# Kernel tuning notes

Measured on AMD Instinct MI355X. Metric: run time of the kernel, lower is better.

## Reference

```python
import jax, jax.numpy as jnp
import numpy as np

H = 32  # hidden size (fixed in source)
V = 95  # input_size == output_size == vocab of chars


def _init_param(key, shape, fan):
    bound = 1.0 / np.sqrt(fan)
    return jax.random.uniform(key, shape, dtype=jnp.float32, minval=-bound, maxval=bound)


def setup_inputs() -> dict:
    key = jax.random.key(0)
    ks = jax.random.split(key, 16)
    B, T = 2048, 256
    inp = {"x": jax.random.normal(ks[0], (B, T, V), dtype=jnp.float32)}
    in_sizes = [V, H, H]
    i = 1
    for l, isz in enumerate(in_sizes, start=1):
        inp[f"Wih{l}"] = _init_param(ks[i], (3 * H, isz), H); i += 1
        inp[f"Whh{l}"] = _init_param(ks[i], (3 * H, H), H); i += 1
        inp[f"bih{l}"] = _init_param(ks[i], (3 * H,), H); i += 1
        inp[f"bhh{l}"] = _init_param(ks[i], (3 * H,), H); i += 1
    inp["Wfc"] = _init_param(ks[13], (V, H), H)
    inp["bfc"] = _init_param(ks[14], (V,), H)
    return inp


def gru_layer(x, Wih, Whh, bih, bhh):
    # x: [B, T, I] -> hs: [B, T, H]; PyTorch GRU gate math, h0 = 0.
    B, T, _ = x.shape
    # Precompute input projections for all timesteps (batched GEMM).
    xp = jnp.einsum('bti,gi->btg', x, Wih) + bih          # [B, T, 3H]
    xr, xz, xn = jnp.split(xp, 3, axis=-1)                # each [B, T, H]
    xs = (jnp.swapaxes(xr, 0, 1), jnp.swapaxes(xz, 0, 1), jnp.swapaxes(xn, 0, 1))
    Whr, Whz, Whn = jnp.split(Whh, 3, axis=0)             # each [H, H]
    bhr, bhz, bhn = jnp.split(bhh, 3, axis=0)

    def step(h, t_in):
        txr, txz, txn = t_in
        r = jax.nn.sigmoid(txr + h @ Whr.T + bhr)
        z = jax.nn.sigmoid(txz + h @ Whz.T + bhz)
        n = jnp.tanh(txn + r * (h @ Whn.T + bhn))
        h_new = (1.0 - z) * n + z * h
        return h_new, h_new

    h0 = jnp.zeros((B, Whh.shape[1]), dtype=x.dtype)
    _, hs = jax.lax.scan(step, h0, xs)                    # hs: [T, B, H]
    return jnp.swapaxes(hs, 0, 1)                         # [B, T, H]


def reference(x, Wih1, Whh1, bih1, bhh1, Wih2, Whh2, bih2, bhh2,
              Wih3, Whh3, bih3, bhh3, Wfc, bfc):
    out = gru_layer(x, Wih1, Whh1, bih1, bhh1)
    out = gru_layer(out, Wih2, Whh2, bih2, bhh2)
    out = gru_layer(out, Wih3, Whh3, bih3, bhh3)
    return jnp.einsum('bth,oh->bto', out, Wfc) + bfc      # [B, T, V]
```

## Files before the change

### kernel.cpp

```cpp
#include <hip/hip_runtime.h>

#define HH 32
#define VV 95
#define TT 256

__device__ __forceinline__ float fast_sigmoid(float v) {
    return __builtin_amdgcn_rcpf(1.0f + __expf(-v));
}
__device__ __forceinline__ float fast_tanh(float v) {
    return 1.0f - 2.0f * __builtin_amdgcn_rcpf(__expf(2.0f * v) + 1.0f);
}
__device__ __forceinline__ void wave_fence() {
    asm volatile("s_waitcnt lgkmcnt(0)" ::: "memory");
    __builtin_amdgcn_wave_barrier();
}

extern "C" __global__ void __launch_bounds__(256, 1) gru_l1(
    const float* __restrict__ x,
    const float* __restrict__ Wih1, const float* __restrict__ Whh1,
    const float* __restrict__ bih1, const float* __restrict__ bhh1,
    float* __restrict__ out)
{
    __shared__ float sW[96 * 95];
    __shared__ float xst[2][8][96];
    __shared__ float hb[8][32];

    const int tid = threadIdx.x;
    for (int i = tid; i < 96 * 95; i += 256) sW[i] = Wih1[i];

    const int s = tid >> 5, j = tid & 31;
    float ur[32], uz[32], un[32];
    #pragma unroll
    for (int k = 0; k < 32; ++k) {
        ur[k] = Whh1[j * 32 + k];
        uz[k] = Whh1[(32 + j) * 32 + k];
        un[k] = Whh1[(64 + j) * 32 + k];
    }
    const float bir = bih1[j], biz = bih1[32 + j], bin_ = bih1[64 + j];
    const float bhr = bhh1[j], bhz = bhh1[32 + j], bhn = bhh1[64 + j];

    const size_t b = (size_t)blockIdx.x * 8 + s;
    const float* xrow = x + b * (size_t)(TT * VV);
    float* orow = out + b * (size_t)(TT * VV);

    hb[s][j] = 0.0f;
    float hj = 0.0f;
    for (int i = j; i < VV; i += 32) xst[0][s][i] = xrow[i];
    __syncthreads();

    const float* wr = sW + j * 95;
    const float* wz = sW + (32 + j) * 95;
    const float* wn = sW + (64 + j) * 95;

    for (int t = 0; t < TT; ++t) {
        const int cur = t & 1;
        float p0 = 0.f, p1 = 0.f, p2 = 0.f;
        if (t + 1 < TT) {
            const float* xn_ = xrow + (t + 1) * VV;
            p0 = xn_[j]; p1 = xn_[32 + j];
            p2 = (j < 31) ? xn_[64 + j] : 0.f;
        }
        const float* xs = xst[cur][s];
        float ar = bir, az = biz, an = bin_;
        #pragma unroll
        for (int i4 = 0; i4 < 23; ++i4) {
            const float4 xv = ((const float4*)xs)[i4];
            const int i = i4 * 4;
            ar = fmaf(wr[i    ], xv.x, ar); az = fmaf(wz[i    ], xv.x, az); an = fmaf(wn[i    ], xv.x, an);
            ar = fmaf(wr[i + 1], xv.y, ar); az = fmaf(wz[i + 1], xv.y, az); an = fmaf(wn[i + 1], xv.y, an);
            ar = fmaf(wr[i + 2], xv.z, ar); az = fmaf(wz[i + 2], xv.z, az); an = fmaf(wn[i + 2], xv.z, an);
            ar = fmaf(wr[i + 3], xv.w, ar); az = fmaf(wz[i + 3], xv.w, az); an = fmaf(wn[i + 3], xv.w, an);
        }
        #pragma unroll
        for (int i = 92; i < 95; ++i) {
            const float xi = xs[i];
            ar = fmaf(wr[i], xi, ar); az = fmaf(wz[i], xi, az); an = fmaf(wn[i], xi, an);
        }
        float hr = bhr, hz = bhz, hn = bhn;
        #pragma unroll
        for (int k = 0; k < 32; ++k) {
            const float hk = hb[s][k];
            hr = fmaf(ur[k], hk, hr); hz = fmaf(uz[k], hk, hz); hn = fmaf(un[k], hk, hn);
        }
        const float r = fast_sigmoid(ar + hr);
        const float z = fast_sigmoid(az + hz);
        const float n = fast_tanh(an + r * hn);
        hj = (1.0f - z) * n + z * hj;

        asm volatile("" ::: "memory");
        hb[s][j] = hj;
        orow[t * 95 + j] = hj;
        if (t + 1 < TT) {
            float* xd = xst[cur ^ 1][s];
            xd[j] = p0; xd[32 + j] = p1;
            if (j < 31) xd[64 + j] = p2;
        }
        wave_fence();
    }
}

extern "C" __global__ void __launch_bounds__(256, 1) gru_l2(
    const float* __restrict__ Wih2, const float* __restrict__ Whh2,
    const float* __restrict__ bih2, const float* __restrict__ bhh2,
    float* __restrict__ out)
{
    __shared__ float ist[2][8][32];
    __shared__ float hb[8][32];
    const int tid = threadIdx.x;
    const int s = tid >> 5, j = tid & 31;

    float vr[32], vz[32], vn[32], ur[32], uz[32], un[32];
    #pragma unroll
    for (int k = 0; k < 32; ++k) {
        vr[k] = Wih2[j * 32 + k];        vz[k] = Wih2[(32 + j) * 32 + k];  vn[k] = Wih2[(64 + j) * 32 + k];
        ur[k] = Whh2[j * 32 + k];        uz[k] = Whh2[(32 + j) * 32 + k];  un[k] = Whh2[(64 + j) * 32 + k];
    }
    const float bir = bih2[j], biz = bih2[32 + j], bin_ = bih2[64 + j];
    const float bhr = bhh2[j], bhz = bhh2[32 + j], bhn = bhh2[64 + j];

    const size_t b = (size_t)blockIdx.x * 8 + s;
    float* orow = out + b * (size_t)(TT * VV);

    hb[s][j] = 0.0f;
    float hj = 0.0f;
    ist[0][s][j] = orow[j];
    wave_fence();

    for (int t = 0; t < TT; ++t) {
        const int cur = t & 1;
        float pn = 0.f;
        if (t + 1 < TT) pn = orow[(t + 1) * 95 + j];

        const float* in = ist[cur][s];
        float ar = bir, az = biz, an = bin_;
        float hr = bhr, hz = bhz, hn = bhn;
        #pragma unroll
        for (int k = 0; k < 32; ++k) {
            const float ik = in[k], hk = hb[s][k];
            ar = fmaf(vr[k], ik, ar); az = fmaf(vz[k], ik, az); an = fmaf(vn[k], ik, an);
            hr = fmaf(ur[k], hk, hr); hz = fmaf(uz[k], hk, hz); hn = fmaf(un[k], hk, hn);
        }
        const float r = fast_sigmoid(ar + hr);
        const float z = fast_sigmoid(az + hz);
        const float n = fast_tanh(an + r * hn);
        hj = (1.0f - z) * n + z * hj;

        orow[t * 95 + 32 + j] = hj;
        asm volatile("" ::: "memory");
        hb[s][j] = hj;
        if (t + 1 < TT) ist[cur ^ 1][s][j] = pn;
        wave_fence();
    }
}

extern "C" __global__ void __launch_bounds__(256, 1) gru_l3fc(
    const float* __restrict__ Wih3, const float* __restrict__ Whh3,
    const float* __restrict__ bih3, const float* __restrict__ bhh3,
    const float* __restrict__ Wfc,  const float* __restrict__ bfc,
    float* __restrict__ out)
{
    __shared__ float ist[2][8][32];
    __shared__ float hb[8][32];
    const int tid = threadIdx.x;
    const int s = tid >> 5, j = tid & 31;

    float vr[32], vz[32], vn[32], ur[32], uz[32], un[32];
    float wf0[32], wf1[32], wf2[32];
    #pragma unroll
    for (int k = 0; k < 32; ++k) {
        vr[k] = Wih3[j * 32 + k];        vz[k] = Wih3[(32 + j) * 32 + k];  vn[k] = Wih3[(64 + j) * 32 + k];
        ur[k] = Whh3[j * 32 + k];        uz[k] = Whh3[(32 + j) * 32 + k];  un[k] = Whh3[(64 + j) * 32 + k];
        wf0[k] = Wfc[j * 32 + k];
        wf1[k] = Wfc[(32 + j) * 32 + k];
        wf2[k] = (j < 31) ? Wfc[(64 + j) * 32 + k] : 0.f;
    }
    const float bir = bih3[j], biz = bih3[32 + j], bin_ = bih3[64 + j];
    const float bhr = bhh3[j], bhz = bhh3[32 + j], bhn = bhh3[64 + j];
    const float bf0 = bfc[j], bf1 = bfc[32 + j], bf2 = (j < 31) ? bfc[64 + j] : 0.f;

    const size_t b = (size_t)blockIdx.x * 8 + s;
    float* orow = out + b * (size_t)(TT * VV);

    hb[s][j] = 0.0f;
    float hj = 0.0f;
    ist[0][s][j] = orow[32 + j];
    wave_fence();

    for (int t = 0; t < TT; ++t) {
        const int cur = t & 1;
        float pn = 0.f;
        if (t + 1 < TT) pn = orow[(t + 1) * 95 + 32 + j];

        const float* in = ist[cur][s];
        float ar = bir, az = biz, an = bin_;
        float hr = bhr, hz = bhz, hn = bhn;
        #pragma unroll
        for (int k = 0; k < 32; ++k) {
            const float ik = in[k], hk = hb[s][k];
            ar = fmaf(vr[k], ik, ar); az = fmaf(vz[k], ik, az); an = fmaf(vn[k], ik, an);
            hr = fmaf(ur[k], hk, hr); hz = fmaf(uz[k], hk, hz); hn = fmaf(un[k], hk, hn);
        }
        const float r = fast_sigmoid(ar + hr);
        const float z = fast_sigmoid(az + hz);
        const float n = fast_tanh(an + r * hn);
        hj = (1.0f - z) * n + z * hj;

        asm volatile("" ::: "memory");
        hb[s][j] = hj;
        wave_fence();

        float o0 = bf0, o1 = bf1, o2 = bf2;
        #pragma unroll
        for (int k = 0; k < 32; ++k) {
            const float hk = hb[s][k];
            o0 = fmaf(wf0[k], hk, o0); o1 = fmaf(wf1[k], hk, o1); o2 = fmaf(wf2[k], hk, o2);
        }
        float* op = orow + t * 95;
        op[j] = o0; op[32 + j] = o1;
        if (j < 31) op[64 + j] = o2;

        asm volatile("" ::: "memory");
        if (t + 1 < TT) ist[cur ^ 1][s][j] = pn;
        wave_fence();
    }
}

extern "C" void kernel_launch(void* const* d_in, const int* in_sizes, int n_in,
                              void* d_out, int out_size, void* d_ws, size_t ws_size,
                              hipStream_t stream) {
    const float* x    = (const float*)d_in[0];
    const float* Wih1 = (const float*)d_in[1];
    const float* Whh1 = (const float*)d_in[2];
    const float* bih1 = (const float*)d_in[3];
    const float* bhh1 = (const float*)d_in[4];
    const float* Wih2 = (const float*)d_in[5];
    const float* Whh2 = (const float*)d_in[6];
    const float* bih2 = (const float*)d_in[7];
    const float* bhh2 = (const float*)d_in[8];
    const float* Wih3 = (const float*)d_in[9];
    const float* Whh3 = (const float*)d_in[10];
    const float* bih3 = (const float*)d_in[11];
    const float* bhh3 = (const float*)d_in[12];
    const float* Wfc  = (const float*)d_in[13];
    const float* bfc  = (const float*)d_in[14];
    float* out = (float*)d_out;

    dim3 grid(256), block(256);
    hipLaunchKernelGGL(gru_l1, grid, block, 0, stream, x, Wih1, Whh1, bih1, bhh1, out);
    hipLaunchKernelGGL(gru_l2, grid, block, 0, stream, Wih2, Whh2, bih2, bhh2, out);
    hipLaunchKernelGGL(gru_l3fc, grid, block, 0, stream, Wih3, Whh3, bih3, bhh3, Wfc, bfc, out);
}
```

Before: 1.054 ms.

## Hoist layer-1 input projection into parallel GEMM and split recurrent dots across half-waves

Adds a separate kernel that computes the layer-1 input projection for all timesteps as a tiled GEMM and writes the first 95 gates into the output buffer. The 96th gate is recomputed inside the recurrence with a wave reduction. Each recurrent kernel now maps one sequence per 64-lane wave: the two half-waves each handle 16 of the 32 hidden inputs, combine partial sums with a lane shuffle, and prefetch two steps ahead. This takes the 95-wide input matmul off the serial critical path and halves per-lane FMA chains, in exchange for an extra kernel launch, extra global traffic for the projected inputs, and shuffle overhead.

```diff
diff --git a/kernel.cpp b/kernel.cpp
--- a/kernel.cpp
+++ b/kernel.cpp
@@ -1,8 +1,7 @@
 #include <hip/hip_runtime.h>
 
-#define HH 32
+#define TT 256
 #define VV 95
-#define TT 256
 
 __device__ __forceinline__ float fast_sigmoid(float v) {
     return __builtin_amdgcn_rcpf(1.0f + __expf(-v));
@@ -15,213 +14,336 @@
     __builtin_amdgcn_wave_barrier();
 }
 
-extern "C" __global__ void __launch_bounds__(256, 1) gru_l1(
-    const float* __restrict__ x,
-    const float* __restrict__ Wih1, const float* __restrict__ Whh1,
-    const float* __restrict__ bih1, const float* __restrict__ bhh1,
-    float* __restrict__ out)
-{
-    __shared__ float sW[96 * 95];
-    __shared__ float xst[2][8][96];
-    __shared__ float hb[8][32];
-
+__device__ __forceinline__ float dot16(const float* w, float4 a, float4 b, float4 c, float4 d) {
+    float s = 0.0f;
+    s = fmaf(w[0],  a.x, s); s = fmaf(w[1],  a.y, s); s = fmaf(w[2],  a.z, s); s = fmaf(w[3],  a.w, s);
+    s = fmaf(w[4],  b.x, s); s = fmaf(w[5],  b.y, s); s = fmaf(w[6],  b.z, s); s = fmaf(w[7],  b.w, s);
+    s = fmaf(w[8],  c.x, s); s = fmaf(w[9],  c.y, s); s = fmaf(w[10], c.z, s); s = fmaf(w[11], c.w, s);
+    s = fmaf(w[12], d.x, s); s = fmaf(w[13], d.y, s); s = fmaf(w[14], d.z, s); s = fmaf(w[15], d.w, s);
+    return s;
+}
+
+__global__ void __launch_bounds__(256) k0_xproj(
+    const float* __restrict__ x, const float* __restrict__ Wih1,
+    const float* __restrict__ bih1, float* __restrict__ out)
+{
+    __shared__ float xs[64 * 98];
+    __shared__ float ws[96 * 98];
     const int tid = threadIdx.x;
-    for (int i = tid; i < 96 * 95; i += 256) sW[i] = Wih1[i];
-
-    const int s = tid >> 5, j = tid & 31;
-    float ur[32], uz[32], un[32];
-    #pragma unroll
-    for (int k = 0; k < 32; ++k) {
-        ur[k] = Whh1[j * 32 + k];
-        uz[k] = Whh1[(32 + j) * 32 + k];
-        un[k] = Whh1[(64 + j) * 32 + k];
-    }
-    const float bir = bih1[j], biz = bih1[32 + j], bin_ = bih1[64 + j];
+    const size_t row0 = (size_t)blockIdx.x * 64;
+
+    const float* xg = x + row0 * VV;
+    for (int i = tid; i < 64 * VV; i += 256) {
+        const int r = i / VV, k = i - r * VV;
+        xs[r * 98 + k] = xg[i];
+    }
+    for (int i = tid; i < 96 * VV; i += 256) {
+        const int g = i / VV, k = i - g * VV;
+        ws[g * 98 + k] = Wih1[i];
+    }
+    if (tid < 64) xs[tid * 98 + VV] = 0.0f;
+    if (tid < 96) ws[tid * 98 + VV] = 0.0f;
+
+    const int rq = tid >> 3;
+    const int gq = tid & 7;
+    float acc[2][12];
+    #pragma unroll
+    for (int c = 0; c < 12; ++c) {
+        const float bv = bih1[gq * 12 + c];
+        acc[0][c] = bv; acc[1][c] = bv;
+    }
+    __syncthreads();
+
+    const float* xr0 = xs + (rq * 2) * 98;
+    const float* xr1 = xr0 + 98;
+    const float* wb_ = ws + (gq * 12) * 98;
+    #pragma unroll 2
+    for (int k2 = 0; k2 < 48; ++k2) {
+        const int k = k2 * 2;
+        const float2 xv0 = *(const float2*)(xr0 + k);
+        const float2 xv1 = *(const float2*)(xr1 + k);
+        #pragma unroll
+        for (int c = 0; c < 12; ++c) {
+            const float2 wv = *(const float2*)(wb_ + c * 98 + k);
+            acc[0][c] = fmaf(wv.x, xv0.x, acc[0][c]);
+            acc[0][c] = fmaf(wv.y, xv0.y, acc[0][c]);
+            acc[1][c] = fmaf(wv.x, xv1.x, acc[1][c]);
+            acc[1][c] = fmaf(wv.y, xv1.y, acc[1][c]);
+        }
+    }
+    #pragma unroll
+    for (int rr = 0; rr < 2; ++rr) {
+        float* orow = out + (row0 + rq * 2 + rr) * VV;
+        #pragma unroll
+        for (int c = 0; c < 12; ++c) {
+            const int g = gq * 12 + c;
+            if (g < VV) orow[g] = acc[rr][c];
+        }
+    }
+}
+
+__device__ __forceinline__ void l1_step(
+    int t, int j, int p, int wid, int i0, int i1,
+    const float* __restrict__ xrow, float* __restrict__ orow, float (*hb)[32],
+    const float* ur, const float* uz, const float* un,
+    float wa, float wb, float bn95, float bhr, float bhz, float bhn,
+    float& hj, float& xr, float& xz, float& xn, float& xa, float& xb)
+{
+    float nr = 0.f, nz = 0.f, nn = 0.f, na = 0.f, nb = 0.f;
+    if (t + 2 < TT) {
+        const float* nx = orow + (t + 2) * VV;
+        nr = nx[j]; nz = nx[32 + j];
+        if (j < 31) nn = nx[64 + j];
+        const float* xx = xrow + (t + 2) * VV;
+        if (i0 < VV) na = xx[i0];
+        if (i1 < VV) nb = xx[i1];
+    }
+    const float4* hv = (const float4*)(&hb[wid][16 * p]);
+    const float4 h0 = hv[0], h1 = hv[1], h2 = hv[2], h3 = hv[3];
+    float hr = dot16(ur, h0, h1, h2, h3);
+    float hz = dot16(uz, h0, h1, h2, h3);
+    float hn = dot16(un, h0, h1, h2, h3);
+    float v = fmaf(wa, xa, wb * xb);
+    v += __shfl_xor(v, 1);  v += __shfl_xor(v, 2);  v += __shfl_xor(v, 4);
+    v += __shfl_xor(v, 8);  v += __shfl_xor(v, 16); v += __shfl_xor(v, 32);
+    const float xnf = (j == 31) ? (v + bn95) : xn;
+    hr += __shfl_xor(hr, 32);
+    hz += __shfl_xor(hz, 32);
+    hn += __shfl_xor(hn, 32);
+    const float r = fast_sigmoid(xr + hr + bhr);
+    const float z = fast_sigmoid(xz + hz + bhz);
+    const float n = fast_tanh(xnf + r * (hn + bhn));
+    hj = (1.0f - z) * n + z * hj;
+    asm volatile("" ::: "memory");
+    if (p == 0) { hb[wid][j] = hj; orow[t * VV + j] = hj; }
+    xr = nr; xz = nz; xn = nn; xa = na; xb = nb;
+    wave_fence();
+}
+
+extern "C" __global__ void __launch_bounds__(256) gru_l1r(
+    const float* __restrict__ x, const float* __restrict__ Wih1,
+    const float* __restrict__ Whh1, const float* __restrict__ bih1,
+    const float* __restrict__ bhh1, float* __restrict__ out)
+{
+    __shared__ __align__(16) float hb[4][32];
+    const int tid = threadIdx.x;
+    const int wid = tid >> 6, l = tid & 63, j = l & 31, p = l >> 5;
+
+    float ur[16], uz[16], un[16];
+    #pragma unroll
+    for (int c = 0; c < 16; ++c) {
+        ur[c] = Whh1[j * 32 + 16 * p + c];
+        uz[c] = Whh1[(32 + j) * 32 + 16 * p + c];
+        un[c] = Whh1[(64 + j) * 32 + 16 * p + c];
+    }
     const float bhr = bhh1[j], bhz = bhh1[32 + j], bhn = bhh1[64 + j];
-
-    const size_t b = (size_t)blockIdx.x * 8 + s;
+    const int i0 = 2 * l, i1 = 2 * l + 1;
+    const float wa = (i0 < VV) ? Wih1[95 * VV + i0] : 0.0f;
+    const float wb = (i1 < VV) ? Wih1[95 * VV + i1] : 0.0f;
+    const float bn95 = bih1[95];
+
+    const size_t b = (size_t)blockIdx.x * 4 + wid;
     const float* xrow = x + b * (size_t)(TT * VV);
     float* orow = out + b * (size_t)(TT * VV);
 
-    hb[s][j] = 0.0f;
+    if (p == 0) hb[wid][j] = 0.0f;
     float hj = 0.0f;
-    for (int i = j; i < VV; i += 32) xst[0][s][i] = xrow[i];
-    __syncthreads();
-
-    const float* wr = sW + j * 95;
-    const float* wz = sW + (32 + j) * 95;
-    const float* wn = sW + (64 + j) * 95;
-
-    for (int t = 0; t < TT; ++t) {
-        const int cur = t & 1;
-        float p0 = 0.f, p1 = 0.f, p2 = 0.f;
-        if (t + 1 < TT) {
-            const float* xn_ = xrow + (t + 1) * VV;
-            p0 = xn_[j]; p1 = xn_[32 + j];
-            p2 = (j < 31) ? xn_[64 + j] : 0.f;
-        }
-        const float* xs = xst[cur][s];
-        float ar = bir, az = biz, an = bin_;
-        #pragma unroll
-        for (int i4 = 0; i4 < 23; ++i4) {
-            const float4 xv = ((const float4*)xs)[i4];
-            const int i = i4 * 4;
-            ar = fmaf(wr[i    ], xv.x, ar); az = fmaf(wz[i    ], xv.x, az); an = fmaf(wn[i    ], xv.x, an);
-            ar = fmaf(wr[i + 1], xv.y, ar); az = fmaf(wz[i + 1], xv.y, az); an = fmaf(wn[i + 1], xv.y, an);
-            ar = fmaf(wr[i + 2], xv.z, ar); az = fmaf(wz[i + 2], xv.z, az); an = fmaf(wn[i + 2], xv.z, an);
-            ar = fmaf(wr[i + 3], xv.w, ar); az = fmaf(wz[i + 3], xv.w, az); an = fmaf(wn[i + 3], xv.w, an);
-        }
-        #pragma unroll
-        for (int i = 92; i < 95; ++i) {
-            const float xi = xs[i];
-            ar = fmaf(wr[i], xi, ar); az = fmaf(wz[i], xi, az); an = fmaf(wn[i], xi, an);
-        }
-        float hr = bhr, hz = bhz, hn = bhn;
-        #pragma unroll
-        for (int k = 0; k < 32; ++k) {
-            const float hk = hb[s][k];
-            hr = fmaf(ur[k], hk, hr); hz = fmaf(uz[k], hk, hz); hn = fmaf(un[k], hk, hn);
-        }
-        const float r = fast_sigmoid(ar + hr);
-        const float z = fast_sigmoid(az + hz);
-        const float n = fast_tanh(an + r * hn);
-        hj = (1.0f - z) * n + z * hj;
-
-        asm volatile("" ::: "memory");
-        hb[s][j] = hj;
-        orow[t * 95 + j] = hj;
-        if (t + 1 < TT) {
-            float* xd = xst[cur ^ 1][s];
-            xd[j] = p0; xd[32 + j] = p1;
-            if (j < 31) xd[64 + j] = p2;
-        }
-        wave_fence();
-    }
-}
-
-extern "C" __global__ void __launch_bounds__(256, 1) gru_l2(
+    float AxR = orow[j], AxZ = orow[32 + j];
+    float AxN = (j < 31) ? orow[64 + j] : 0.f;
+    float AxA = (i0 < VV) ? xrow[i0] : 0.f;
+    float AxB = (i1 < VV) ? xrow[i1] : 0.f;
+    const float* r1 = orow + VV; const float* x1 = xrow + VV;
+    float BxR = r1[j], BxZ = r1[32 + j];
+    float BxN = (j < 31) ? r1[64 + j] : 0.f;
+    float BxA = (i0 < VV) ? x1[i0] : 0.f;
+    float BxB = (i1 < VV) ? x1[i1] : 0.f;
+    wave_fence();
+
+    for (int t = 0; t < TT; t += 2) {
+        l1_step(t,     j, p, wid, i0, i1, xrow, orow, hb, ur, uz, un,
+                wa, wb, bn95, bhr, bhz, bhn, hj, AxR, AxZ, AxN, AxA, AxB);
+        l1_step(t + 1, j, p, wid, i0, i1, xrow, orow, hb, ur, uz, un,
+                wa, wb, bn95, bhr, bhz, bhn, hj, BxR, BxZ, BxN, BxA, BxB);
+    }
+}
+
+__device__ __forceinline__ void l2_step(
+    int t, int j, int p, int wid,
+    float* __restrict__ orow, float (*hb)[32], float (*ist)[4][32],
+    const float* vr, const float* vz, const float* vn,
+    const float* ur, const float* uz, const float* un,
+    float br, float bz, float bni, float bnh,
+    float& hj, float& pn)
+{
+    float pnN = (t + 3 < TT) ? orow[(t + 3) * VV + j] : 0.f;
+    const int cur = t & 1;
+    const float4* iv = (const float4*)(&ist[cur][wid][16 * p]);
+    const float4 a0 = iv[0], a1 = iv[1], a2 = iv[2], a3 = iv[3];
+    const float4* hv = (const float4*)(&hb[wid][16 * p]);
+    const float4 h0 = hv[0], h1 = hv[1], h2 = hv[2], h3 = hv[3];
+    float ar = dot16(vr, a0, a1, a2, a3);
+    float az = dot16(vz, a0, a1, a2, a3);
+    float an = dot16(vn, a0, a1, a2, a3);
+    float hr = dot16(ur, h0, h1, h2, h3);
+    float hz = dot16(uz, h0, h1, h2, h3);
+    float hn = dot16(un, h0, h1, h2, h3);
+    float s1 = ar + hr; s1 += __shfl_xor(s1, 32);
+    float s2 = az + hz; s2 += __shfl_xor(s2, 32);
+    an += __shfl_xor(an, 32);
+    hn += __shfl_xor(hn, 32);
+    const float r = fast_sigmoid(s1 + br);
+    const float z = fast_sigmoid(s2 + bz);
+    const float n = fast_tanh(an + bni + r * (hn + bnh));
+    hj = (1.0f - z) * n + z * hj;
+    asm volatile("" ::: "memory");
+    if (p == 0) {
+        hb[wid][j] = hj;
+        orow[t * VV + 32 + j] = hj;
+        ist[cur ^ 1][wid][j] = pn;
+    }
+    pn = pnN;
+    wave_fence();
+}
+
+extern "C" __global__ void __launch_bounds__(256) gru_l2r(
     const float* __restrict__ Wih2, const float* __restrict__ Whh2,
     const float* __restrict__ bih2, const float* __restrict__ bhh2,
     float* __restrict__ out)
 {
-    __shared__ float ist[2][8][32];
-    __shared__ float hb[8][32];
+    __shared__ __align__(16) float hb[4][32];
+    __shared__ __align__(16) float ist[2][4][32];
     const int tid = threadIdx.x;
-    const int s = tid >> 5, j = tid & 31;
-
-    float vr[32], vz[32], vn[32], ur[32], uz[32], un[32];
-    #pragma unroll
-    for (int k = 0; k < 32; ++k) {
-        vr[k] = Wih2[j * 32 + k];        vz[k] = Wih2[(32 + j) * 32 + k];  vn[k] = Wih2[(64 + j) * 32 + k];
-        ur[k] = Whh2[j * 32 + k];        uz[k] = Whh2[(32 + j) * 32 + k];  un[k] = Whh2[(64 + j) * 32 + k];
-    }
-    const float bir = bih2[j], biz = bih2[32 + j], bin_ = bih2[64 + j];
-    const float bhr = bhh2[j], bhz = bhh2[32 + j], bhn = bhh2[64 + j];
-
-    const size_t b = (size_t)blockIdx.x * 8 + s;
+    const int wid = tid >> 6, l = tid & 63, j = l & 31, p = l >> 5;
+
+    float vr[16], vz[16], vn[16], ur[16], uz[16], un[16];
+    #pragma unroll
+    for (int c = 0; c < 16; ++c) {
+        vr[c] = Wih2[j * 32 + 16 * p + c];
+        vz[c] = Wih2[(32 + j) * 32 + 16 * p + c];
+        vn[c] = Wih2[(64 + j) * 32 + 16 * p + c];
+        ur[c] = Whh2[j * 32 + 16 * p + c];
+        uz[c] = Whh2[(32 + j) * 32 + 16 * p + c];
+        un[c] = Whh2[(64 + j) * 32 + 16 * p + c];
+    }
+    const float br = bih2[j] + bhh2[j];
+    const float bz = bih2[32 + j] + bhh2[32 + j];
+    const float bni = bih2[64 + j], bnh = bhh2[64 + j];
+
+    const size_t b = (size_t)blockIdx.x * 4 + wid;
     float* orow = out + b * (size_t)(TT * VV);
 
-    hb[s][j] = 0.0f;
+    if (p == 0) { hb[wid][j] = 0.0f; ist[0][wid][j] = orow[j]; }
     float hj = 0.0f;
-    ist[0][s][j] = orow[j];
-    wave_fence();
-
-    for (int t = 0; t < TT; ++t) {
-        const int cur = t & 1;
-        float pn = 0.f;
-        if (t + 1 < TT) pn = orow[(t + 1) * 95 + j];
-
-        const float* in = ist[cur][s];
-        float ar = bir, az = biz, an = bin_;
-        float hr = bhr, hz = bhz, hn = bhn;
-        #pragma unroll
-        for (int k = 0; k < 32; ++k) {
-            const float ik = in[k], hk = hb[s][k];
-            ar = fmaf(vr[k], ik, ar); az = fmaf(vz[k], ik, az); an = fmaf(vn[k], ik, an);
-            hr = fmaf(ur[k], hk, hr); hz = fmaf(uz[k], hk, hz); hn = fmaf(un[k], hk, hn);
-        }
-        const float r = fast_sigmoid(ar + hr);
-        const float z = fast_sigmoid(az + hz);
-        const float n = fast_tanh(an + r * hn);
-        hj = (1.0f - z) * n + z * hj;
-
-        orow[t * 95 + 32 + j] = hj;
-        asm volatile("" ::: "memory");
-        hb[s][j] = hj;
-        if (t + 1 < TT) ist[cur ^ 1][s][j] = pn;
-        wave_fence();
-    }
-}
-
-extern "C" __global__ void __launch_bounds__(256, 1) gru_l3fc(
+    float pnA = orow[1 * VV + j];
+    float pnB = orow[2 * VV + j];
+    wave_fence();
+
+    for (int t = 0; t < TT; t += 2) {
+        l2_step(t,     j, p, wid, orow, hb, ist, vr, vz, vn, ur, uz, un,
+                br, bz, bni, bnh, hj, pnA);
+        l2_step(t + 1, j, p, wid, orow, hb, ist, vr, vz, vn, ur, uz, un,
+                br, bz, bni, bnh, hj, pnB);
+    }
+}
+
+__device__ __forceinline__ void l3_step(
+    int t, int j, int p, int wid,
+    float* __restrict__ orow, float (*hb)[32], float (*ist)[4][32],
+    const float* vr, const float* vz, const float* vn,
+    const float* ur, const float* uz, const float* un,
+    const float* wf0, const float* wf1, const float* wf2,
+    float br, float bz, float bni, float bnh,
+    float bf0, float bf1, float bf2,
+    float& hj, float& pn)
+{
+    float pnN = (t + 3 < TT) ? orow[(t + 3) * VV + 32 + j] : 0.f;
+    const int cur = t & 1;
+    const float4* iv = (const float4*)(&ist[cur][wid][16 * p]);
+    const float4 a0 = iv[0], a1 = iv[1], a2 = iv[2], a3 = iv[3];
+    const float4* hv = (const float4*)(&hb[wid][16 * p]);
+    const float4 h0 = hv[0], h1 = hv[1], h2 = hv[2], h3 = hv[3];
+    float ar = dot16(vr, a0, a1, a2, a3);
+    float az = dot16(vz, a0, a1, a2, a3);
+    float an = dot16(vn, a0, a1, a2, a3);
+    float hr = dot16(ur, h0, h1, h2, h3);
+    float hz = dot16(uz, h0, h1, h2, h3);
+    float hn = dot16(un, h0, h1, h2, h3);
+    float s1 = ar + hr; s1 += __shfl_xor(s1, 32);
+    float s2 = az + hz; s2 += __shfl_xor(s2, 32);
+    an += __shfl_xor(an, 32);
+    hn += __shfl_xor(hn, 32);
+    const float r = fast_sigmoid(s1 + br);
+    const float z = fast_sigmoid(s2 + bz);
+    const float n = fast_tanh(an + bni + r * (hn + bnh));
+    hj = (1.0f - z) * n + z * hj;
+    asm volatile("" ::: "memory");
+    if (p == 0) hb[wid][j] = hj;
+    wave_fence();
+    const float4* gv = (const float4*)(&hb[wid][16 * p]);
+    const float4 g0 = gv[0], g1 = gv[1], g2 = gv[2], g3 = gv[3];
+    float o0 = dot16(wf0, g0, g1, g2, g3);
+    float o1 = dot16(wf1, g0, g1, g2, g3);
+    float o2 = dot16(wf2, g0, g1, g2, g3);
+    o0 += __shfl_xor(o0, 32);
+    o1 += __shfl_xor(o1, 32);
+    o2 += __shfl_xor(o2, 32);
+    asm volatile("" ::: "memory");
+    if (p == 0) {
+        float* op = orow + t * VV;
+        op[j] = o0 + bf0;
+        op[32 + j] = o1 + bf1;
+        if (j < 31) op[64 + j] = o2 + bf2;
+        ist[cur ^ 1][wid][j] = pn;
+    }
+    pn = pnN;
+    wave_fence();
+}
+
+extern "C" __global__ void __launch_bounds__(256) gru_l3fc(
     const float* __restrict__ Wih3, const float* __restrict__ Whh3,
     const float* __restrict__ bih3, const float* __restrict__ bhh3,
     const float* __restrict__ Wfc,  const float* __restrict__ bfc,
     float* __restrict__ out)
 {
-    __shared__ float ist[2][8][32];
-    __shared__ float hb[8][32];
+    __shared__ __align__(16) float hb[4][32];
+    __shared__ __align__(16) float ist[2][4][32];
     const int tid = threadIdx.x;
-    const int s = tid >> 5, j = tid & 31;
-
-    float vr[32], vz[32], vn[32], ur[32], uz[32], un[32];
-    float wf0[32], wf1[32], wf2[32];
-    #pragma unroll
-    for (int k = 0; k < 32; ++k) {
-        vr[k] = Wih3[j * 32 + k];        vz[k] = Wih3[(32 + j) * 32 + k];  vn[k] = Wih3[(64 + j) * 32 + k];
-        ur[k] = Whh3[j * 32 + k];        uz[k] = Whh3[(32 + j) * 32 + k];  un[k] = Whh3[(64 + j) * 32 + k];
-        wf0[k] = Wfc[j * 32 + k];
-        wf1[k] = Wfc[(32 + j) * 32 + k];
-        wf2[k] = (j < 31) ? Wfc[(64 + j) * 32 + k] : 0.f;
-    }
-    const float bir = bih3[j], biz = bih3[32 + j], bin_ = bih3[64 + j];
-    const float bhr = bhh3[j], bhz = bhh3[32 + j], bhn = bhh3[64 + j];
-    const float bf0 = bfc[j], bf1 = bfc[32 + j], bf2 = (j < 31) ? bfc[64 + j] : 0.f;
-
-    const size_t b = (size_t)blockIdx.x * 8 + s;
+    const int wid = tid >> 6, l = tid & 63, j = l & 31, p = l >> 5;
+
+    float vr[16], vz[16], vn[16], ur[16], uz[16], un[16];
+    float wf0[16], wf1[16], wf2[16];
+    #pragma unroll
+    for (int c = 0; c < 16; ++c) {
+        vr[c] = Wih3[j * 32 + 16 * p + c];
+        vz[c] = Wih3[(32 + j) * 32 + 16 * p + c];
+        vn[c] = Wih3[(64 + j) * 32 + 16 * p + c];
+        ur[c] = Whh3[j * 32 + 16 * p + c];
+        uz[c] = Whh3[(32 + j) * 32 + 16 * p + c];
+        un[c] = Whh3[(64 + j) * 32 + 16 * p + c];
+        wf0[c] = Wfc[j * 32 + 16 * p + c];
+        wf1[c] = Wfc[(32 + j) * 32 + 16 * p + c];
+        wf2[c] = (j < 31) ? Wfc[(64 + j) * 32 + 16 * p + c] : 0.f;
+    }
+    const float br = bih3[j] + bhh3[j];
+    const float bz = bih3[32 + j] + bhh3[32 + j];
+    const float bni = bih3[64 + j], bnh = bhh3[64 + j];
+    const float bf0 = bfc[j], bf1 = bfc[32 + j];
+    const float bf2 = (j < 31) ? bfc[64 + j] : 0.f;
+
+    const size_t b = (size_t)blockIdx.x * 4 + wid;
     float* orow = out + b * (size_t)(TT * VV);
 
-    hb[s][j] = 0.0f;
+    if (p == 0) { hb[wid][j] = 0.0f; ist[0][wid][j] = orow[32 + j]; }
     float hj = 0.0f;
-    ist[0][s][j] = orow[32 + j];
-    wave_fence();
-
-    for (int t = 0; t < TT; ++t) {
-        const int cur = t & 1;
-        float pn = 0.f;
-        if (t + 1 < TT) pn = orow[(t + 1) * 95 + 32 + j];
-
-        const float* in = ist[cur][s];
-        float ar = bir, az = biz, an = bin_;
-        float hr = bhr, hz = bhz, hn = bhn;
-        #pragma unroll
-        for (int k = 0; k < 32; ++k) {
-            const float ik = in[k], hk = hb[s][k];
-            ar = fmaf(vr[k], ik, ar); az = fmaf(vz[k], ik, az); an = fmaf(vn[k], ik, an);
-            hr = fmaf(ur[k], hk, hr); hz = fmaf(uz[k], hk, hz); hn = fmaf(un[k], hk, hn);
-        }
-        const float r = fast_sigmoid(ar + hr);
-        const float z = fast_sigmoid(az + hz);
-        const float n = fast_tanh(an + r * hn);
-        hj = (1.0f - z) * n + z * hj;
-
-        asm volatile("" ::: "memory");
-        hb[s][j] = hj;
-        wave_fence();
-
-        float o0 = bf0, o1 = bf1, o2 = bf2;
-        #pragma unroll
-        for (int k = 0; k < 32; ++k) {
-            const float hk = hb[s][k];
-            o0 = fmaf(wf0[k], hk, o0); o1 = fmaf(wf1[k], hk, o1); o2 = fmaf(wf2[k], hk, o2);
-        }
-        float* op = orow + t * 95;
-        op[j] = o0; op[32 + j] = o1;
-        if (j < 31) op[64 + j] = o2;
-
-        asm volatile("" ::: "memory");
-        if (t + 1 < TT) ist[cur ^ 1][s][j] = pn;
-        wave_fence();
+    float pnA = orow[1 * VV + 32 + j];
+    float pnB = orow[2 * VV + 32 + j];
+    wave_fence();
+
+    for (int t = 0; t < TT; t += 2) {
+        l3_step(t,     j, p, wid, orow, hb, ist, vr, vz, vn, ur, uz, un,
+                wf0, wf1, wf2, br, bz, bni, bnh, bf0, bf1, bf2, hj, pnA);
+        l3_step(t + 1, j, p, wid, orow, hb, ist, vr, vz, vn, ur, uz, un,
+                wf0, wf1, wf2, br, bz, bni, bnh, bf0, bf1, bf2, hj, pnB);
     }
 }
 
@@ -245,8 +367,8 @@
     const float* bfc  = (const float*)d_in[14];
     float* out = (float*)d_out;
 
-    dim3 grid(256), block(256);
-    hipLaunchKernelGGL(gru_l1, grid, block, 0, stream, x, Wih1, Whh1, bih1, bhh1, out);
-    hipLaunchKernelGGL(gru_l2, grid, block, 0, stream, Wih2, Whh2, bih2, bhh2, out);
-    hipLaunchKernelGGL(gru_l3fc, grid, block, 0, stream, Wih3, Whh3, bih3, bhh3, Wfc, bfc, out);
-}
+    hipLaunchKernelGGL(k0_xproj, dim3(8192), dim3(256), 0, stream, x, Wih1, bih1, out);
+    hipLaunchKernelGGL(gru_l1r,  dim3(512),  dim3(256), 0, stream, x, Wih1, Whh1, bih1, bhh1, out);
+    hipLaunchKernelGGL(gru_l2r,  dim3(512),  dim3(256), 0, stream, Wih2, Whh2, bih2, bhh2, out);
+    hipLaunchKernelGGL(gru_l3fc, dim3(512),  dim3(256), 0, stream, Wih3, Whh3, bih3, bhh3, Wfc, bfc, out);
+}
```

Result: faster. 929.5 us (-11.8%).
